# Kernel tuning notes

Hardware: AMD Instinct MI355X
Metric: run time of the kernel (lower is better)

## Reference

```python
import jax, jax.numpy as jnp
import numpy as np

B, T, D, H = 4, 2048, 384, 6
HD = D // H  # 64
HALF = HD // 2


def setup_inputs() -> dict:
    key = jax.random.key(0)
    k0, k1, k2 = jax.random.split(key, 3)
    x = jax.random.normal(k0, (B, T, D), jnp.float32)
    attn_bias = jnp.zeros((1, 1, T, T), jnp.float32)  # additive SDPA bias
    # standard RoPE tables: [T, HD/2]
    inv_freq = 1.0 / (10000.0 ** (np.arange(HALF, dtype=np.float32) / HALF))
    ang = np.arange(T, dtype=np.float32)[:, None] * inv_freq[None, :]
    cos = jnp.asarray(np.cos(ang), jnp.float32)
    sin = jnp.asarray(np.sin(ang), jnp.float32)
    w_qkv = jax.random.normal(k1, (D, 3 * D), jnp.float32) * (D ** -0.5)
    w_proj = jax.random.normal(k2, (D, D), jnp.float32) * (D ** -0.5)
    return {"x": x, "attn_bias": attn_bias, "cos": cos, "sin": sin,
            "w_qkv": w_qkv, "w_proj": w_proj}


def _apply_rope(x, cos, sin):
    # x: [b, h, t, hd]; cos/sin: [t, hd/2] -> rotate-half RoPE
    half = x.shape[-1] // 2
    x1, x2 = x[..., :half], x[..., half:]
    c = cos[None, None, :, :]
    s = sin[None, None, :, :]
    return jnp.concatenate([x1 * c - x2 * s, x2 * c + x1 * s], axis=-1)


def reference(x, attn_bias, cos, sin, w_qkv, w_proj):
    b, t, _ = x.shape
    qkv = (x @ w_qkv).reshape(b, t, 3, H, HD)  # fused QKV projection
    q = jnp.transpose(qkv[:, :, 0], (0, 2, 1, 3))  # [b,h,t,hd]
    k = jnp.transpose(qkv[:, :, 1], (0, 2, 1, 3))
    v = jnp.transpose(qkv[:, :, 2], (0, 2, 1, 3))
    q = _apply_rope(q, cos, sin)
    k = _apply_rope(k, cos, sin)
    scale = 1.0 / jnp.sqrt(jnp.asarray(HD, x.dtype))
    scores = jnp.einsum("bhqd,bhkd->bhqk", q, k) * scale + attn_bias
    attn = jax.nn.softmax(scores, axis=-1)
    out = jnp.einsum("bhqk,bhkd->bhqd", attn, v)
    out = jnp.transpose(out, (0, 2, 1, 3)).reshape(b, t, H * HD)
    return out @ w_proj
```

## Files before the change

kernel.cpp:

```cpp
#include <hip/hip_runtime.h>
#include <hip/hip_bf16.h>

#define BB   4
#define TT   2048
#define DDIM 384
#define HH   6
#define HD   64
#define BT   (BB*TT)
#define QKVC (3*DDIM)

typedef __attribute__((ext_vector_type(4))) short short4v;
typedef __attribute__((ext_vector_type(8))) short short8v;
typedef __attribute__((ext_vector_type(4))) float float4v;
typedef unsigned short u16;

static __device__ __forceinline__ u16 f2bu(float f) {
    __hip_bfloat16 h = __float2bfloat16(f);
    return __builtin_bit_cast(u16, h);
}

static __device__ __forceinline__ short8v ld_frag(const u16* p) {
    short4v a = *(const short4v*)p;
    short4v b = *(const short4v*)(p + 4);
    return __builtin_shufflevector(a, b, 0, 1, 2, 3, 4, 5, 6, 7);
}

static __device__ __forceinline__ void st8(u16* p, uint4 v) {
    *(uint2*)p       = make_uint2(v.x, v.y);
    *(uint2*)(p + 4) = make_uint2(v.z, v.w);
}

#define MFMA16(a, b, c) __builtin_amdgcn_mfma_f32_16x16x32_bf16((a), (b), (c), 0, 0, 0)

__global__ __launch_bounds__(256) void prep_kernel(
    const float* __restrict__ wqkv, const float* __restrict__ wproj,
    u16* __restrict__ wqkvT, u16* __restrict__ wprojT)
{
    const int bid = blockIdx.x;
    const int t = threadIdx.x;
    const float* in; u16* out; int K, C, c0, k0;
    if (bid < 108) { in = wqkv;  out = wqkvT;  K = DDIM; C = QKVC;
                     c0 = (bid % 18) * 64; k0 = (bid / 18) * 64; }
    else           { int b2 = bid - 108; in = wproj; out = wprojT; K = DDIM; C = DDIM;
                     c0 = (b2 % 6) * 64; k0 = (b2 / 6) * 64; }
    __shared__ float tr[64][65];
    {
        int kr = t >> 2, cb = (t & 3) * 16;
        const float* gp = in + (size_t)(k0 + kr) * C + c0 + cb;
        #pragma unroll
        for (int u = 0; u < 4; ++u) {
            float4 v = *(const float4*)(gp + 4 * u);
            tr[cb + 4 * u + 0][kr] = v.x;
            tr[cb + 4 * u + 1][kr] = v.y;
            tr[cb + 4 * u + 2][kr] = v.z;
            tr[cb + 4 * u + 3][kr] = v.w;
        }
    }
    __syncthreads();
    {
        int c = t >> 2, kb = (t & 3) * 16;
        __align__(16) u16 tmp[16];
        #pragma unroll
        for (int u = 0; u < 16; ++u) tmp[u] = f2bu(tr[c][kb + u]);
        u16* op = out + (size_t)(c0 + c) * K + k0 + kb;
        *(uint4*)op       = *(const uint4*)tmp;
        *(uint4*)(op + 8) = *(const uint4*)(tmp + 8);
    }
}

__global__ __launch_bounds__(256) void qkv_rope_kernel(
    const float* __restrict__ x, const u16* __restrict__ wt,
    const float* __restrict__ cs, const float* __restrict__ sn,
    u16* __restrict__ qb, u16* __restrict__ kb, u16* __restrict__ vtb)
{
    __shared__ __align__(16) u16 as_[128][68];
    __shared__ __align__(16) u16 bs_[128][68];
    const int t = threadIdx.x;
    const int wv = t >> 6, lane = t & 63, quad = lane >> 4, lo = lane & 15;
    const int wy = wv >> 1, wx = wv & 1;
    const int r0 = blockIdx.y * 128;
    const int c0 = blockIdx.x * 128;
    const int arow = t >> 1, ak = (t & 1) * 32;

    float4v acc[4][4] = {};

    for (int kk = 0; kk < 6; ++kk) {
        if (kk) __syncthreads();
        {
            const float* gp = x + (size_t)(r0 + arow) * DDIM + kk * 64 + ak;
            #pragma unroll
            for (int u = 0; u < 4; ++u) {
                float4 v0 = *(const float4*)(gp + 8 * u);
                float4 v1 = *(const float4*)(gp + 8 * u + 4);
                uint4 pk;
                pk.x = f2bu(v0.x) | ((unsigned)f2bu(v0.y) << 16);
                pk.y = f2bu(v0.z) | ((unsigned)f2bu(v0.w) << 16);
                pk.z = f2bu(v1.x) | ((unsigned)f2bu(v1.y) << 16);
                pk.w = f2bu(v1.z) | ((unsigned)f2bu(v1.w) << 16);
                st8(&as_[arow][ak + 8 * u], pk);
            }
        }
        {
            const u16* wp = wt + (size_t)(c0 + arow) * DDIM + kk * 64 + ak;
            #pragma unroll
            for (int u = 0; u < 4; ++u)
                st8(&bs_[arow][ak + 8 * u], *(const uint4*)(wp + 8 * u));
        }
        __syncthreads();

        #pragma unroll
        for (int kf = 0; kf < 2; ++kf) {
            short8v af[4];
            #pragma unroll
            for (int rt = 0; rt < 4; ++rt)
                af[rt] = ld_frag(&as_[64 * wy + 16 * rt + lo][kf * 32 + quad * 8]);
            #pragma unroll
            for (int ct = 0; ct < 4; ++ct) {
                short8v bf = ld_frag(&bs_[64 * wx + 16 * ct + lo][kf * 32 + quad * 8]);
                #pragma unroll
                for (int rt = 0; rt < 4; ++rt)
                    acc[rt][ct] = MFMA16(af[rt], bf, acc[rt][ct]);
            }
        }
    }

    const int sec  = c0 / DDIM;
    const int h    = (c0 % DDIM) / HD + wx;
    const int bidx = r0 >> 11;

    #pragma unroll
    for (int rt = 0; rt < 4; ++rt) {
        const int tbase = (r0 + 64 * wy + 16 * rt + 4 * quad) & (TT - 1);
        if (sec == 2) {
            #pragma unroll
            for (int ct = 0; ct < 4; ++ct) {
                int d = ct * 16 + lo;
                unsigned a0 = f2bu(acc[rt][ct][0]) | ((unsigned)f2bu(acc[rt][ct][1]) << 16);
                unsigned a1 = f2bu(acc[rt][ct][2]) | ((unsigned)f2bu(acc[rt][ct][3]) << 16);
                u16* gp = vtb + ((size_t)(bidx * HH + h) * HD + d) * TT + tbase;
                *(uint2*)gp = make_uint2(a0, a1);
            }
        } else {
            u16* dst = (sec == 0) ? qb : kb;
            #pragma unroll
            for (int np = 0; np < 2; ++np) {
                #pragma unroll
                for (int r = 0; r < 4; ++r) {
                    int tpos = tbase + r;
                    int ci = np * 16 + lo;
                    float cv = cs[tpos * 32 + ci];
                    float sv = sn[tpos * 32 + ci];
                    float x1 = acc[rt][np][r], x2 = acc[rt][np + 2][r];
                    unsigned pk = f2bu(x1 * cv - x2 * sv) |
                                  ((unsigned)f2bu(x2 * cv + x1 * sv) << 16);
                    unsigned* gp = (unsigned*)(dst +
                        ((size_t)(bidx * HH + h) * TT + tpos) * HD);
                    gp[ci] = pk;
                }
            }
        }
    }
}

__global__ __launch_bounds__(256, 3) void attn_kernel(
    const u16* __restrict__ qb, const u16* __restrict__ kb, const u16* __restrict__ vtb,
    const float* __restrict__ bias, u16* __restrict__ ob)
{
    __shared__ __align__(16) u16 ks[2][64][68];
    __shared__ __align__(16) u16 vt[2][64][68];
    __shared__ __align__(16) u16 ps[4][16][68];

    const int t = threadIdx.x;
    const int wv = t >> 6, lane = t & 63, quad = lane >> 4, lo = lane & 15;
    const int bh = blockIdx.y;
    const int b = bh / HH, h = bh % HH;
    const int q0 = blockIdx.x * 64;
    const int qrow = q0 + 16 * wv + 4 * quad;

    const u16* qbase = qb + ((size_t)bh * TT + q0 + 16 * wv + lo) * HD + quad * 8;
    short8v aq[2];
    aq[0] = __builtin_bit_cast(short8v, *(const uint4*)qbase);
    aq[1] = __builtin_bit_cast(short8v, *(const uint4*)(qbase + 32));

    const int sr = t >> 3, sd = (t & 7) * 8;
    const u16* kbbase = kb + (size_t)bh * TT * HD;
    const u16* vtbase = vtb + (size_t)bh * HD * TT;

    st8(&ks[0][sr][sd],      *(const uint4*)(kbbase + (size_t)sr * HD + sd));
    st8(&ks[0][sr + 32][sd], *(const uint4*)(kbbase + (size_t)(sr + 32) * HD + sd));
    st8(&vt[0][sr][sd],      *(const uint4*)(vtbase + (size_t)sr * TT + sd));
    st8(&vt[0][sr + 32][sd], *(const uint4*)(vtbase + (size_t)(sr + 32) * TT + sd));
    float bcur[4][4];
    #pragma unroll
    for (int nt = 0; nt < 4; ++nt)
        #pragma unroll
        for (int r = 0; r < 4; ++r)
            bcur[nt][r] = bias[(size_t)(qrow + r) * TT + nt * 16 + lo];
    __syncthreads();

    float4v oacc[4] = {};
    float lacc[4] = {0.f, 0.f, 0.f, 0.f};

    for (int kt = 0; kt < TT / 64; ++kt) {
        const int cur = kt & 1, nxt = cur ^ 1;
        const int kn = (kt < 31 ? kt + 1 : 31) * 64;

        uint4 kp0 = *(const uint4*)(kbbase + (size_t)(kn + sr) * HD + sd);
        uint4 kp1 = *(const uint4*)(kbbase + (size_t)(kn + sr + 32) * HD + sd);
        uint4 vp0 = *(const uint4*)(vtbase + (size_t)sr * TT + kn + sd);
        uint4 vp1 = *(const uint4*)(vtbase + (size_t)(sr + 32) * TT + kn + sd);
        float bnxt[4][4];
        #pragma unroll
        for (int nt = 0; nt < 4; ++nt)
            #pragma unroll
            for (int r = 0; r < 4; ++r)
                bnxt[nt][r] = bias[(size_t)(qrow + r) * TT + kn + nt * 16 + lo];

        float4v s[4] = {};
        #pragma unroll
        for (int kf = 0; kf < 2; ++kf) {
            #pragma unroll
            for (int nt = 0; nt < 4; ++nt) {
                short8v bfr = ld_frag(&ks[cur][nt * 16 + lo][kf * 32 + quad * 8]);
                s[nt] = MFMA16(aq[kf], bfr, s[nt]);
            }
        }

        #pragma unroll
        for (int nt = 0; nt < 4; ++nt)
            #pragma unroll
            for (int r = 0; r < 4; ++r) {
                float p = __expf(s[nt][r] * 0.125f + bcur[nt][r]);
                lacc[r] += p;
                ps[wv][4 * quad + r][nt * 16 + lo] = f2bu(p);
            }

        #pragma unroll
        for (int kf = 0; kf < 2; ++kf) {
            short8v ap = ld_frag(&ps[wv][lo][kf * 32 + quad * 8]);
            #pragma unroll
            for (int nt = 0; nt < 4; ++nt) {
                short8v bv = ld_frag(&vt[cur][nt * 16 + lo][kf * 32 + quad * 8]);
                oacc[nt] = MFMA16(ap, bv, oacc[nt]);
            }
        }

        st8(&ks[nxt][sr][sd], kp0);
        st8(&ks[nxt][sr + 32][sd], kp1);
        st8(&vt[nxt][sr][sd], vp0);
        st8(&vt[nxt][sr + 32][sd], vp1);
        #pragma unroll
        for (int nt = 0; nt < 4; ++nt)
            #pragma unroll
            for (int r = 0; r < 4; ++r)
                bcur[nt][r] = bnxt[nt][r];
        __syncthreads();
    }

    #pragma unroll
    for (int r = 0; r < 4; ++r) {
        float l = lacc[r];
        l += __shfl_xor(l, 1);
        l += __shfl_xor(l, 2);
        l += __shfl_xor(l, 4);
        l += __shfl_xor(l, 8);
        float inv = 1.f / l;
        u16* gp = ob + ((size_t)b * TT + qrow + r) * DDIM + h * HD;
        #pragma unroll
        for (int nt = 0; nt < 4; ++nt)
            gp[nt * 16 + lo] = f2bu(oacc[nt][r] * inv);
    }
}

__global__ __launch_bounds__(256) void proj_kernel(
    const u16* __restrict__ o, const u16* __restrict__ wt, float* __restrict__ out)
{
    __shared__ __align__(16) u16 os[2][64][68];
    __shared__ __align__(16) u16 ws[2][64][68];
    const int t = threadIdx.x;
    const int wv = t >> 6, lane = t & 63, quad = lane >> 4, lo = lane & 15;
    const int r0 = blockIdx.y * 64, c0 = blockIdx.x * 64;
    const int sr = t >> 3, sd = (t & 7) * 8;

    st8(&os[0][sr][sd],      *(const uint4*)(o + (size_t)(r0 + sr) * DDIM + sd));
    st8(&os[0][sr + 32][sd], *(const uint4*)(o + (size_t)(r0 + sr + 32) * DDIM + sd));
    st8(&ws[0][sr][sd],      *(const uint4*)(wt + (size_t)(c0 + sr) * DDIM + sd));
    st8(&ws[0][sr + 32][sd], *(const uint4*)(wt + (size_t)(c0 + sr + 32) * DDIM + sd));
    __syncthreads();

    float4v acc[4] = {};
    for (int kk = 0; kk < 6; ++kk) {
        const int cur = kk & 1, nxt = cur ^ 1;
        const int kkn = (kk < 5 ? kk + 1 : 5) * 64;
        uint4 op0 = *(const uint4*)(o + (size_t)(r0 + sr) * DDIM + kkn + sd);
        uint4 op1 = *(const uint4*)(o + (size_t)(r0 + sr + 32) * DDIM + kkn + sd);
        uint4 wp0 = *(const uint4*)(wt + (size_t)(c0 + sr) * DDIM + kkn + sd);
        uint4 wp1 = *(const uint4*)(wt + (size_t)(c0 + sr + 32) * DDIM + kkn + sd);

        #pragma unroll
        for (int kf = 0; kf < 2; ++kf) {
            short8v a = ld_frag(&os[cur][16 * wv + lo][kf * 32 + quad * 8]);
            #pragma unroll
            for (int nt = 0; nt < 4; ++nt) {
                short8v bfr = ld_frag(&ws[cur][nt * 16 + lo][kf * 32 + quad * 8]);
                acc[nt] = MFMA16(a, bfr, acc[nt]);
            }
        }
        st8(&os[nxt][sr][sd], op0);
        st8(&os[nxt][sr + 32][sd], op1);
        st8(&ws[nxt][sr][sd], wp0);
        st8(&ws[nxt][sr + 32][sd], wp1);
        __syncthreads();
    }
    #pragma unroll
    for (int r = 0; r < 4; ++r) {
        float* gp = out + (size_t)(r0 + 16 * wv + 4 * quad + r) * DDIM + c0;
        #pragma unroll
        for (int nt = 0; nt < 4; ++nt)
            gp[nt * 16 + lo] = acc[nt][r];
    }
}

extern "C" void kernel_launch(void* const* d_in, const int* in_sizes, int n_in,
                              void* d_out, int out_size, void* d_ws, size_t ws_size,
                              hipStream_t stream) {
    const float* x     = (const float*)d_in[0];
    const float* bias  = (const float*)d_in[1];
    const float* cs    = (const float*)d_in[2];
    const float* sn    = (const float*)d_in[3];
    const float* wqkv  = (const float*)d_in[4];
    const float* wproj = (const float*)d_in[5];
    float* out = (float*)d_out;

    u16* wqkvT  = (u16*)d_ws;
    u16* wprojT = wqkvT + (size_t)QKVC * DDIM;
    u16* qb     = wprojT + (size_t)DDIM * DDIM;
    u16* kb     = qb + (size_t)BB * HH * TT * HD;
    u16* vtb    = kb + (size_t)BB * HH * TT * HD;
    u16* ob     = vtb + (size_t)BB * HH * TT * HD;

    prep_kernel<<<dim3(144), 256, 0, stream>>>(wqkv, wproj, wqkvT, wprojT);
    qkv_rope_kernel<<<dim3(QKVC / 128, BT / 128), 256, 0, stream>>>(
        x, wqkvT, cs, sn, qb, kb, vtb);
    attn_kernel<<<dim3(TT / 64, BB * HH), 256, 0, stream>>>(
        qb, kb, vtb, bias, ob);
    proj_kernel<<<dim3(DDIM / 64, BT / 64), 256, 0, stream>>>(ob, wprojT, out);
}
```

Baseline: 184.1 us.

## Split attention keys across waves, compute transposed scores, and pre-convert bias to bf16

The attention kernel changes from giving each wave 16 query rows to giving each wave 16 key columns of every 64-key tile for all 64 queries. Scores are computed transposed (K as the A operand), so P is used straight from registers in a 16x16x16 MFMA against V with no LDS round trip for P. Partial outputs and row sums are reduced across the four waves through LDS at the end. The additive bias is converted to bf16 in the prep kernel, which halves bias traffic in the attention loop but adds a full TxT conversion pass and rounds the bias to bf16. Each thread now keeps 64 output accumulators, which raises register pressure under the 3-blocks-per-SM launch bound.

Result: slower. 195.0 us (+5.9%).

```diff
diff --git a/kernel.cpp b/kernel.cpp
--- a/kernel.cpp
+++ b/kernel.cpp
@@ -18,6 +18,10 @@
     __hip_bfloat16 h = __float2bfloat16(f);
     return __builtin_bit_cast(u16, h);
 }
+static __device__ __forceinline__ float bu2f(u16 v) {
+    unsigned u = (unsigned)v << 16;
+    return __builtin_bit_cast(float, u);
+}
 
 static __device__ __forceinline__ short8v ld_frag(const u16* p) {
     short4v a = *(const short4v*)p;
@@ -32,12 +36,33 @@
 
 #define MFMA16(a, b, c) __builtin_amdgcn_mfma_f32_16x16x32_bf16((a), (b), (c), 0, 0, 0)
 
+#if __has_builtin(__builtin_amdgcn_mfma_f32_16x16x16_bf16)
+#define MFMAK16(a, b, c) __builtin_amdgcn_mfma_f32_16x16x16_bf16((a), (b), (c), 0, 0, 0)
+#else
+#define MFMAK16(a, b, c) __builtin_amdgcn_mfma_f32_16x16x16bf16_1k((a), (b), (c), 0, 0, 0)
+#endif
+
 __global__ __launch_bounds__(256) void prep_kernel(
     const float* __restrict__ wqkv, const float* __restrict__ wproj,
-    u16* __restrict__ wqkvT, u16* __restrict__ wprojT)
+    const float* __restrict__ bias,
+    u16* __restrict__ wqkvT, u16* __restrict__ wprojT, u16* __restrict__ biasb)
 {
     const int bid = blockIdx.x;
     const int t = threadIdx.x;
+    if (bid >= 144) {
+        size_t base = (size_t)(bid - 144) * 4096 + (size_t)t * 16;
+        const float* gp = bias + base;
+        __align__(16) u16 tmp[16];
+        #pragma unroll
+        for (int u = 0; u < 4; ++u) {
+            float4 v = *(const float4*)(gp + 4 * u);
+            tmp[4 * u + 0] = f2bu(v.x); tmp[4 * u + 1] = f2bu(v.y);
+            tmp[4 * u + 2] = f2bu(v.z); tmp[4 * u + 3] = f2bu(v.w);
+        }
+        *(uint4*)(biasb + base)     = *(const uint4*)tmp;
+        *(uint4*)(biasb + base + 8) = *(const uint4*)(tmp + 8);
+        return;
+    }
     const float* in; u16* out; int K, C, c0, k0;
     if (bid < 108) { in = wqkv;  out = wqkvT;  K = DDIM; C = QKVC;
                      c0 = (bid % 18) * 64; k0 = (bid / 18) * 64; }
@@ -164,41 +189,42 @@
 
 __global__ __launch_bounds__(256, 3) void attn_kernel(
     const u16* __restrict__ qb, const u16* __restrict__ kb, const u16* __restrict__ vtb,
-    const float* __restrict__ bias, u16* __restrict__ ob)
+    const u16* __restrict__ biasb, u16* __restrict__ ob)
 {
-    __shared__ __align__(16) u16 ks[2][64][68];
-    __shared__ __align__(16) u16 vt[2][64][68];
-    __shared__ __align__(16) u16 ps[4][16][68];
+    __shared__ __align__(16) u16 smem[2 * 2 * 64 * 72];
+    __shared__ float lred[4][64];
+    u16 (*ks)[64][72] = (u16(*)[64][72])smem;
+    u16 (*vt)[64][72] = (u16(*)[64][72])(smem + 2 * 64 * 72);
 
     const int t = threadIdx.x;
     const int wv = t >> 6, lane = t & 63, quad = lane >> 4, lo = lane & 15;
     const int bh = blockIdx.y;
     const int b = bh / HH, h = bh % HH;
     const int q0 = blockIdx.x * 64;
-    const int qrow = q0 + 16 * wv + 4 * quad;
-
-    const u16* qbase = qb + ((size_t)bh * TT + q0 + 16 * wv + lo) * HD + quad * 8;
-    short8v aq[2];
-    aq[0] = __builtin_bit_cast(short8v, *(const uint4*)qbase);
-    aq[1] = __builtin_bit_cast(short8v, *(const uint4*)(qbase + 32));
+
+    short8v aq[4][2];
+    #pragma unroll
+    for (int s = 0; s < 4; ++s) {
+        const u16* qp = qb + ((size_t)bh * TT + q0 + 16 * s + lo) * HD + quad * 8;
+        aq[s][0] = __builtin_bit_cast(short8v, *(const uint4*)qp);
+        aq[s][1] = __builtin_bit_cast(short8v, *(const uint4*)(qp + 32));
+    }
 
     const int sr = t >> 3, sd = (t & 7) * 8;
     const u16* kbbase = kb + (size_t)bh * TT * HD;
     const u16* vtbase = vtb + (size_t)bh * HD * TT;
-
-    st8(&ks[0][sr][sd],      *(const uint4*)(kbbase + (size_t)sr * HD + sd));
-    st8(&ks[0][sr + 32][sd], *(const uint4*)(kbbase + (size_t)(sr + 32) * HD + sd));
-    st8(&vt[0][sr][sd],      *(const uint4*)(vtbase + (size_t)sr * TT + sd));
-    st8(&vt[0][sr + 32][sd], *(const uint4*)(vtbase + (size_t)(sr + 32) * TT + sd));
-    float bcur[4][4];
-    #pragma unroll
-    for (int nt = 0; nt < 4; ++nt)
-        #pragma unroll
-        for (int r = 0; r < 4; ++r)
-            bcur[nt][r] = bias[(size_t)(qrow + r) * TT + nt * 16 + lo];
+    const u16* bp = biasb + (size_t)(q0 + lo) * TT + 16 * wv + 4 * quad;
+
+    *(uint4*)&ks[0][sr][sd]      = *(const uint4*)(kbbase + (size_t)sr * HD + sd);
+    *(uint4*)&ks[0][sr + 32][sd] = *(const uint4*)(kbbase + (size_t)(sr + 32) * HD + sd);
+    *(uint4*)&vt[0][sr][sd]      = *(const uint4*)(vtbase + (size_t)sr * TT + sd);
+    *(uint4*)&vt[0][sr + 32][sd] = *(const uint4*)(vtbase + (size_t)(sr + 32) * TT + sd);
+    uint2 pb[4];
+    #pragma unroll
+    for (int s = 0; s < 4; ++s) pb[s] = *(const uint2*)(bp + (size_t)s * 16 * TT);
     __syncthreads();
 
-    float4v oacc[4] = {};
+    float4v oacc[4][4] = {};
     float lacc[4] = {0.f, 0.f, 0.f, 0.f};
 
     for (int kt = 0; kt < TT / 64; ++kt) {
@@ -209,66 +235,104 @@
         uint4 kp1 = *(const uint4*)(kbbase + (size_t)(kn + sr + 32) * HD + sd);
         uint4 vp0 = *(const uint4*)(vtbase + (size_t)sr * TT + kn + sd);
         uint4 vp1 = *(const uint4*)(vtbase + (size_t)(sr + 32) * TT + kn + sd);
-        float bnxt[4][4];
-        #pragma unroll
-        for (int nt = 0; nt < 4; ++nt)
-            #pragma unroll
-            for (int r = 0; r < 4; ++r)
-                bnxt[nt][r] = bias[(size_t)(qrow + r) * TT + kn + nt * 16 + lo];
-
-        float4v s[4] = {};
-        #pragma unroll
-        for (int kf = 0; kf < 2; ++kf) {
-            #pragma unroll
-            for (int nt = 0; nt < 4; ++nt) {
-                short8v bfr = ld_frag(&ks[cur][nt * 16 + lo][kf * 32 + quad * 8]);
-                s[nt] = MFMA16(aq[kf], bfr, s[nt]);
-            }
-        }
-
-        #pragma unroll
-        for (int nt = 0; nt < 4; ++nt)
-            #pragma unroll
-            for (int r = 0; r < 4; ++r) {
-                float p = __expf(s[nt][r] * 0.125f + bcur[nt][r]);
-                lacc[r] += p;
-                ps[wv][4 * quad + r][nt * 16 + lo] = f2bu(p);
-            }
-
-        #pragma unroll
-        for (int kf = 0; kf < 2; ++kf) {
-            short8v ap = ld_frag(&ps[wv][lo][kf * 32 + quad * 8]);
-            #pragma unroll
-            for (int nt = 0; nt < 4; ++nt) {
-                short8v bv = ld_frag(&vt[cur][nt * 16 + lo][kf * 32 + quad * 8]);
-                oacc[nt] = MFMA16(ap, bv, oacc[nt]);
-            }
-        }
-
-        st8(&ks[nxt][sr][sd], kp0);
-        st8(&ks[nxt][sr + 32][sd], kp1);
-        st8(&vt[nxt][sr][sd], vp0);
-        st8(&vt[nxt][sr + 32][sd], vp1);
-        #pragma unroll
-        for (int nt = 0; nt < 4; ++nt)
-            #pragma unroll
-            for (int r = 0; r < 4; ++r)
-                bcur[nt][r] = bnxt[nt][r];
+        uint2 pbn[4];
+        #pragma unroll
+        for (int s = 0; s < 4; ++s)
+            pbn[s] = *(const uint2*)(bp + kn + (size_t)s * 16 * TT);
+
+        short8v ka0 = __builtin_bit_cast(short8v,
+            *(const uint4*)&ks[cur][16 * wv + lo][quad * 8]);
+        short8v ka1 = __builtin_bit_cast(short8v,
+            *(const uint4*)&ks[cur][16 * wv + lo][32 + quad * 8]);
+
+        float4v sv[4];
+        #pragma unroll
+        for (int s = 0; s < 4; ++s) {
+            float4v z = {};
+            sv[s] = MFMA16(ka0, aq[s][0], z);
+            sv[s] = MFMA16(ka1, aq[s][1], sv[s]);
+        }
+
+        short4v pa[4];
+        #pragma unroll
+        for (int s = 0; s < 4; ++s) {
+            float b0 = bu2f((u16)(pb[s].x & 0xffff));
+            float b1 = bu2f((u16)(pb[s].x >> 16));
+            float b2 = bu2f((u16)(pb[s].y & 0xffff));
+            float b3 = bu2f((u16)(pb[s].y >> 16));
+            float p0 = __expf(fmaf(sv[s][0], 0.125f, b0));
+            float p1 = __expf(fmaf(sv[s][1], 0.125f, b1));
+            float p2 = __expf(fmaf(sv[s][2], 0.125f, b2));
+            float p3 = __expf(fmaf(sv[s][3], 0.125f, b3));
+            lacc[s] += (p0 + p1) + (p2 + p3);
+            short4v pvv = { (short)f2bu(p0), (short)f2bu(p1),
+                            (short)f2bu(p2), (short)f2bu(p3) };
+            pa[s] = pvv;
+        }
+
+        short4v vb[4];
+        #pragma unroll
+        for (int dt = 0; dt < 4; ++dt)
+            vb[dt] = *(const short4v*)&vt[cur][16 * dt + lo][16 * wv + 4 * quad];
+
+        #pragma unroll
+        for (int s = 0; s < 4; ++s)
+            #pragma unroll
+            for (int dt = 0; dt < 4; ++dt)
+                oacc[s][dt] = MFMAK16(pa[s], vb[dt], oacc[s][dt]);
+
+        *(uint4*)&ks[nxt][sr][sd]      = kp0;
+        *(uint4*)&ks[nxt][sr + 32][sd] = kp1;
+        *(uint4*)&vt[nxt][sr][sd]      = vp0;
+        *(uint4*)&vt[nxt][sr + 32][sd] = vp1;
+        #pragma unroll
+        for (int s = 0; s < 4; ++s) pb[s] = pbn[s];
         __syncthreads();
     }
 
     #pragma unroll
-    for (int r = 0; r < 4; ++r) {
-        float l = lacc[r];
-        l += __shfl_xor(l, 1);
-        l += __shfl_xor(l, 2);
-        l += __shfl_xor(l, 4);
-        l += __shfl_xor(l, 8);
-        float inv = 1.f / l;
-        u16* gp = ob + ((size_t)b * TT + qrow + r) * DDIM + h * HD;
-        #pragma unroll
-        for (int nt = 0; nt < 4; ++nt)
-            gp[nt * 16 + lo] = f2bu(oacc[nt][r] * inv);
+    for (int s = 0; s < 4; ++s) {
+        lacc[s] += __shfl_xor(lacc[s], 16);
+        lacc[s] += __shfl_xor(lacc[s], 32);
+    }
+    if (quad == 0) {
+        #pragma unroll
+        for (int s = 0; s < 4; ++s) lred[wv][s * 16 + lo] = lacc[s];
+    }
+    float (*obuf)[16][68] = (float(*)[16][68])smem;
+    #pragma unroll
+    for (int dt = 0; dt < 4; ++dt)
+        #pragma unroll
+        for (int r = 0; r < 4; ++r)
+            obuf[wv][4 * quad + r][16 * dt + lo] = oacc[0][dt][r];
+    __syncthreads();
+
+    const int i = t >> 4, j4 = (t & 15) * 4;
+    #pragma unroll
+    for (int s = 0; s < 4; ++s) {
+        float4 s0 = *(const float4*)&obuf[0][i][j4];
+        float4 s1 = *(const float4*)&obuf[1][i][j4];
+        float4 s2 = *(const float4*)&obuf[2][i][j4];
+        float4 s3 = *(const float4*)&obuf[3][i][j4];
+        float inv = 1.f / (lred[0][s * 16 + i] + lred[1][s * 16 + i] +
+                           lred[2][s * 16 + i] + lred[3][s * 16 + i]);
+        float o0 = (s0.x + s1.x + s2.x + s3.x) * inv;
+        float o1 = (s0.y + s1.y + s2.y + s3.y) * inv;
+        float o2 = (s0.z + s1.z + s2.z + s3.z) * inv;
+        float o3 = (s0.w + s1.w + s2.w + s3.w) * inv;
+        unsigned a0 = f2bu(o0) | ((unsigned)f2bu(o1) << 16);
+        unsigned a1 = f2bu(o2) | ((unsigned)f2bu(o3) << 16);
+        u16* gp = ob + ((size_t)b * TT + q0 + 16 * s + i) * DDIM + h * HD + j4;
+        *(uint2*)gp = make_uint2(a0, a1);
+        __syncthreads();
+        if (s < 3) {
+            #pragma unroll
+            for (int dt = 0; dt < 4; ++dt)
+                #pragma unroll
+                for (int r = 0; r < 4; ++r)
+                    obuf[wv][4 * quad + r][16 * dt + lo] = oacc[s + 1][dt][r];
+            __syncthreads();
+        }
     }
 }
 
@@ -338,11 +402,13 @@
     u16* kb     = qb + (size_t)BB * HH * TT * HD;
     u16* vtb    = kb + (size_t)BB * HH * TT * HD;
     u16* ob     = vtb + (size_t)BB * HH * TT * HD;
-
-    prep_kernel<<<dim3(144), 256, 0, stream>>>(wqkv, wproj, wqkvT, wprojT);
+    u16* biasb  = ob + (size_t)BT * DDIM;
+
+    prep_kernel<<<dim3(144 + 1024), 256, 0, stream>>>(
+        wqkv, wproj, bias, wqkvT, wprojT, biasb);
     qkv_rope_kernel<<<dim3(QKVC / 128, BT / 128), 256, 0, stream>>>(
         x, wqkvT, cs, sn, qb, kb, vtb);
     attn_kernel<<<dim3(TT / 64, BB * HH), 256, 0, stream>>>(
-        qb, kb, vtb, bias, ob);
+        qb, kb, vtb, biasb, ob);
     proj_kernel<<<dim3(DDIM / 64, BT / 64), 256, 0, stream>>>(ob, wprojT, out);
 }
```
